# Kernel tuning notes

Hardware: AMD Instinct MI355X
Metric: run time of the kernel (lower is better)

Reference implementation:

```python
import jax, jax.numpy as jnp
import numpy as np

# ---- model hyperparameters (match init_kwargs) ----
N_ATOMS = 16000
N_EDGES = 256000
F = 128          # n_atom_basis
NF = 32          # n_filters
L = 3            # n_interactions
N_RBF = 20
CUTOFF = 5.0
MAX_Z = 100
INV_SQRT_F = np.float32(1.0 / np.sqrt(F))
INV_SQRT_2NF = np.float32(1.0 / np.sqrt(2 * NF))
SQ2 = np.float32(np.sqrt(2.0)); SQ3 = np.float32(np.sqrt(3.0)); SQ6 = np.float32(np.sqrt(6.0))
LOG2 = np.float32(np.log(2.0))


def ssp(x):
    # shifted softplus: softplus(x) - log(2)
    return jax.nn.softplus(x) - LOG2


def setup_inputs() -> dict:
    key = jax.random.key(0)
    k = jax.random.split(key, 16)
    Z = jax.random.randint(k[0], (N_ATOMS,), 0, MAX_Z)
    r_ij = jax.random.normal(k[1], (N_EDGES, 3), dtype=jnp.float32) * 2.0
    idx_i = jnp.sort(jax.random.randint(k[2], (N_EDGES,), 0, N_ATOMS))
    idx_j = jax.random.randint(k[3], (N_EDGES,), 0, N_ATOMS)
    # parameters (e3nn Linear: N(0,1) weights with explicit 1/sqrt(fan_in) in the math;
    # filter-network Dense: fan-in scaled weights, zero bias; padding_idx=0 -> zero row)
    emb = jax.random.normal(k[4], (MAX_Z, F), dtype=jnp.float32).at[0].set(0.0)
    W_pe = jax.random.normal(k[5], (F, F), dtype=jnp.float32)
    W0s = jax.random.normal(k[6], (L, F, NF), dtype=jnp.float32)   # in2f, 0e path
    W0v = jax.random.normal(k[7], (L, F, NF), dtype=jnp.float32)   # in2f, 1o path
    Wf1 = jax.random.normal(k[8], (L, N_RBF, NF), dtype=jnp.float32) / np.sqrt(N_RBF)
    bf1 = jnp.zeros((L, NF), jnp.float32)
    Wf2 = jax.random.normal(k[9], (L, NF, 6 * NF), dtype=jnp.float32) / np.sqrt(NF)
    bf2 = jnp.zeros((L, 6 * NF), jnp.float32)
    As = jax.random.normal(k[10], (L, 2 * NF, F), dtype=jnp.float32)  # f2out_1 0e
    Av = jax.random.normal(k[11], (L, 2 * NF, F), dtype=jnp.float32)  # f2out_1 1o
    Bs = jax.random.normal(k[12], (L, F, F), dtype=jnp.float32)       # f2out_2 0e
    Bv = jax.random.normal(k[13], (L, F, F), dtype=jnp.float32)       # f2out_2 1o
    return dict(Z=Z, r_ij=r_ij, idx_i=idx_i, idx_j=idx_j, emb=emb, W_pe=W_pe,
                W0s=W0s, W0v=W0v, Wf1=Wf1, bf1=bf1, Wf2=Wf2, bf2=bf2,
                As=As, Av=Av, Bs=Bs, Bv=Bv)


def _interaction(xs, xv, idx_i, idx_j, f_ij, rcut, Yv,
                 W0s, W0v, Wf1, bf1, Wf2, bf2, As, Av, Bs, Bv):
    n_atoms = xs.shape[0]
    # in2f: e3nn o3.Linear (per-l channel mixing, fan-in normalized)
    hs = (xs @ W0s) * INV_SQRT_F                        # [N, NF]  (0e)
    hv = jnp.einsum('nfc,fg->ngc', xv, W0v) * INV_SQRT_F  # [N, NF, 3] (1o)
    sj = hs[idx_j]                                      # gather neighbors [E, NF]
    vj = hv[idx_j]                                      # [E, NF, 3]
    # FullTensorProduct (0e+1o) x Y(0e+1o); Y0 = 1, Y1 = sqrt(3)*r_hat (component norm)
    Yb = Yv[:, None, :]                                 # [E, 1, 3]
    t0a = sj                                            # 0e x 0e -> 0e
    t0b = jnp.einsum('efc,ec->ef', vj, Yv) / SQ3        # 1o x 1o -> 0e
    t1a = sj[:, :, None] * Yb                           # 0e x 1o -> 1o
    t1b = vj                                            # 1o x 0e -> 1o
    t1e = jnp.cross(vj, Yb) / SQ2                       # 1o x 1o -> 1e
    ux, uy, uz = vj[..., 0], vj[..., 1], vj[..., 2]
    wx, wy, wz = Yv[:, None, 0], Yv[:, None, 1], Yv[:, None, 2]
    t2e = jnp.stack([(ux * wy + uy * wx) / SQ2,         # 1o x 1o -> 2e (sym traceless)
                     (uy * wz + uz * wy) / SQ2,
                     (2 * uz * wz - ux * wx - uy * wy) / SQ6,
                     (ux * wz + uz * wx) / SQ2,
                     (ux * wx - uy * wy) / SQ2], axis=-1)  # [E, NF, 5]
    # filter network + cutoff envelope: W_ij [E, 6*NF] (one scalar per irrep)
    W = (ssp(f_ij @ Wf1 + bf1) @ Wf2 + bf2) * rcut[:, None]
    w0a, w0b, w1a, w1b, w1e, w2e = jnp.split(W, 6, axis=1)
    E = sj.shape[0]
    # elementwise tensor product (scale each irrep by its scalar), then scatter-add
    y_all = jnp.concatenate([
        t0a * w0a, t0b * w0b,
        (t1a * w1a[..., None]).reshape(E, -1),
        (t1b * w1b[..., None]).reshape(E, -1),
        (t1e * w1e[..., None]).reshape(E, -1),
        (t2e * w2e[..., None]).reshape(E, -1)], axis=1)   # [E, 16*NF]
    agg = jax.ops.segment_sum(y_all, idx_i, num_segments=n_atoms)  # [N, 16*NF]
    s_in = agg[:, :2 * NF]
    v_in = agg[:, 2 * NF:8 * NF].reshape(n_atoms, 2 * NF, 3)
    # f2out_1: output irreps are F x (0e+1o) -> 1e and 2e channels have no path (dropped)
    os = ssp((s_in @ As) * INV_SQRT_2NF)                # f2out_1 + scalar activation
    ov = jnp.einsum('nfc,fg->ngc', v_in, Av) * INV_SQRT_2NF
    os = (os @ Bs) * INV_SQRT_F                         # f2out_2
    ov = jnp.einsum('nfc,fg->ngc', ov, Bv) * INV_SQRT_F
    return os, ov


def _forward(Z, r_ij, idx_i, idx_j, emb, W_pe, W0s, W0v, Wf1, bf1, Wf2, bf2, As, Av, Bs, Bv):
    xs = (emb[Z] @ W_pe) * INV_SQRT_F                   # embedding + post_embedding (0e)
    xv = jnp.zeros((xs.shape[0], F, 3), xs.dtype)       # 1o part starts at zero (no 0e->1o path)
    d = jnp.linalg.norm(r_ij, axis=1)
    offsets = jnp.linspace(0.0, CUTOFF, N_RBF).astype(jnp.float32)
    coeff = -0.5 / (offsets[1] - offsets[0]) ** 2
    f_ij = jnp.exp(coeff * (d[:, None] - offsets) ** 2)  # Gaussian RBF [E, N_RBF]
    rcut = 0.5 * (jnp.cos(np.float32(np.pi) * d / CUTOFF) + 1.0) * (d < CUTOFF)
    # spherical harmonics, normalize=True + component normalization (Y0=1, Y1=sqrt(3)*rhat);
    # the r_ij*rcut prescaling in the original doesn't change the direction, and edges with
    # rcut=0 contribute nothing since W_ij carries the rcut factor.
    Yv = SQ3 * r_ij / jnp.maximum(d, 1e-9)[:, None]
    for l in range(L):
        vs, vv = _interaction(xs, xv, idx_i, idx_j, f_ij, rcut, Yv,
                              W0s[l], W0v[l], Wf1[l], bf1[l], Wf2[l], bf2[l],
                              As[l], Av[l], Bs[l], Bv[l])
        xs = xs + vs
        xv = xv + vv
    return xs  # scalar_representation [N, F]


def reference(Z, r_ij, idx_i, idx_j, emb, W_pe, W0s, W0v, Wf1, bf1, Wf2, bf2, As, Av, Bs, Bv):
    return _forward(Z, r_ij, idx_i, idx_j, emb, W_pe, W0s, W0v, Wf1, bf1, Wf2, bf2, As, Av, Bs, Bv)
```

## Files before the change

### kernel.cpp

```cpp
#include <hip/hip_runtime.h>
#include <math.h>

constexpr int NA   = 16000;
constexpr int NE   = 256000;
constexpr int F    = 128;
constexpr int NF   = 32;
constexpr int NRBF = 20;
constexpr float CUTOFF       = 5.0f;
constexpr float INV_SQRT_F   = 0.0883883476483184f;
constexpr float INV_SQRT_2NF = 0.125f;
constexpr float INV_SQ3      = 0.5773502691896258f;
constexpr float SQ3          = 1.7320508075688772f;
constexpr float LOG2_        = 0.6931471805599453f;
constexpr float PI_          = 3.14159265358979323f;

typedef _Float16 h2 __attribute__((ext_vector_type(2)));

__device__ __forceinline__ float ssp(float x) {
    return fmaxf(x, 0.0f) + __logf(1.0f + __expf(-fabsf(x))) - LOG2_;
}
__device__ __forceinline__ float fdot2(h2 a, h2 b, float c) {
#if __has_builtin(__builtin_amdgcn_fdot2)
    return __builtin_amdgcn_fdot2(a, b, c, false);
#else
    return c + (float)a[0]*(float)b[0] + (float)a[1]*(float)b[1];
#endif
}

__global__ void geom_kernel(const float* __restrict__ r_ij,
                            float* __restrict__ fijT,
                            float* __restrict__ yvrT) {
    int e = blockIdx.x * blockDim.x + threadIdx.x;
    if (e >= NE) return;
    float x = r_ij[3*e+0], y = r_ij[3*e+1], z = r_ij[3*e+2];
    float d = sqrtf(x*x + y*y + z*z);
    const float delta = CUTOFF / (NRBF - 1);
    const float coeff = -0.5f / (delta * delta);
    #pragma unroll
    for (int k = 0; k < NRBF; k++) {
        float t = d - delta * (float)k;
        fijT[(size_t)k*NE + e] = __expf(coeff * t * t);
    }
    float rc = 0.5f * (__cosf(PI_ * d / CUTOFF) + 1.0f);
    rc = (d < CUTOFF) ? rc : 0.0f;
    float inv = SQ3 / fmaxf(d, 1e-9f);
    yvrT[0*(size_t)NE + e] = x * inv;
    yvrT[1*(size_t)NE + e] = y * inv;
    yvrT[2*(size_t)NE + e] = z * inv;
    yvrT[3*(size_t)NE + e] = rc;
}

__global__ void preph_kernel(const float* __restrict__ Wf2, const float* __restrict__ Wf1,
                             h2* __restrict__ Wf2H, h2* __restrict__ Wf1H) {
    int u = blockIdx.x * 256 + threadIdx.x;
    if (u < 3*128*16) {
        int l = u / (128*16), rem = u % (128*16), c = rem >> 4, k2 = rem & 15;
        const float* W = Wf2 + (size_t)l*NF*192;
        Wf2H[u] = h2{(_Float16)W[(2*k2)*192 + c], (_Float16)W[(2*k2+1)*192 + c]};
    }
    if (u < 3*320) {
        int l = u / 320, rem = u % 320, k2 = rem >> 5, g = rem & 31;
        const float* W = Wf1 + (size_t)l*NRBF*NF;
        Wf1H[u] = h2{(_Float16)W[(2*k2)*32 + g], (_Float16)W[(2*k2+1)*32 + g]};
    }
}

__global__ void prep2_kernel(const float* __restrict__ Av, const float* __restrict__ Bv,
                             float* __restrict__ AvBv) {
    int u = blockIdx.x * 256 + threadIdx.x;
    if (u >= 3*64*128) return;
    int l = u >> 13, rem = u & 8191, f = rem >> 7, c = rem & 127;
    const float* av = Av + (size_t)l*64*128 + f*128;
    const float* bv = Bv + (size_t)l*128*128 + c;
    float acc = 0.f;
    #pragma unroll 8
    for (int g = 0; g < 128; g++) acc += av[g] * bv[(size_t)g*128];
    AvBv[u] = acc * (INV_SQRT_2NF * INV_SQRT_F);
}

__global__ __launch_bounds__(256, 4)
void embed_kernel(const int* __restrict__ Z,
                  const float* __restrict__ emb,
                  const float* __restrict__ Wpe,
                  const float* __restrict__ W0s,
                  float* __restrict__ xs,
                  float* __restrict__ hsv) {
    __shared__ float ER[32][128];
    __shared__ int   Zs[32];
    int t = threadIdx.x;
    int a0 = blockIdx.x * 32;
    if (t < 32) Zs[t] = Z[a0 + t];
    __syncthreads();
    {
        const float4* emb4 = (const float4*)emb;
        float4* ER4 = (float4*)&ER[0][0];
        #pragma unroll
        for (int it = 0; it < 4; it++) {
            int u4 = it*256 + t;
            int a = u4 >> 5, k4 = u4 & 31;
            ER4[u4] = emb4[(size_t)Zs[a]*32 + k4];
        }
    }
    __syncthreads();
    int c = t & 127, half = t >> 7;
    float acc[16];
    #pragma unroll
    for (int a = 0; a < 16; a++) acc[a] = 0.f;
    for (int k = 0; k < 128; k++) {
        float w = Wpe[k*128 + c];
        #pragma unroll
        for (int a = 0; a < 16; a++) acc[a] += ER[half*16 + a][k] * w;
    }
    __syncthreads();
    #pragma unroll
    for (int a = 0; a < 16; a++) {
        float v = acc[a] * INV_SQRT_F;
        xs[(size_t)(a0 + half*16 + a)*128 + c] = v;
        ER[half*16 + a][c] = v;
    }
    __syncthreads();
    {
        int g = t & 31, rr = t >> 5;
        float a2[4] = {0.f, 0.f, 0.f, 0.f};
        for (int k = 0; k < 128; k++) {
            float w = W0s[k*32 + g];
            #pragma unroll
            for (int a = 0; a < 4; a++) a2[a] += ER[rr*4 + a][k] * w;
        }
        #pragma unroll
        for (int a = 0; a < 4; a++)
            hsv[(size_t)(a0 + rr*4 + a)*128 + g] = a2[a] * INV_SQRT_F;
        for (int u = t; u < 32*96; u += 256) {
            int a = u / 96, rem = u - a*96;
            hsv[(size_t)(a0 + a)*128 + 32 + rem] = 0.f;
        }
    }
}

__global__ __launch_bounds__(256, 4)
void h_kernel(const float* __restrict__ xs,
              const float* __restrict__ xv,
              const float* __restrict__ W0s,
              const float* __restrict__ W0v,
              float* __restrict__ hsv) {
    __shared__ float X[16][512];
    int t = threadIdx.x;
    int a0 = blockIdx.x * 16;
    {
        float* Xf = &X[0][0];
        const float4* xs4 = (const float4*)xs;
        const float4* xv4 = (const float4*)xv;
        #pragma unroll
        for (int it = 0; it < 2; it++) {
            int u4 = it*256 + t;
            int a = u4 >> 5, k4 = u4 & 31;
            *(float4*)&Xf[a*512 + k4*4] = xs4[(size_t)a0*32 + u4];
        }
        #pragma unroll
        for (int it = 0; it < 6; it++) {
            int u4 = it*256 + t;
            int a = u4 / 96, rem = u4 - a*96;
            *(float4*)&Xf[a*512 + 128 + rem*4] = xv4[(size_t)a0*96 + u4];
        }
    }
    __syncthreads();
    int g = t & 31, r = t >> 5;
    int sel = r & 3, half = r >> 2;
    const float* W = (sel == 0) ? W0s : W0v;
    int xoff = (sel == 0) ? 0 : (128 + (sel-1)*128);
    float acc[8];
    #pragma unroll
    for (int a = 0; a < 8; a++) acc[a] = 0.f;
    for (int k = 0; k < 128; k++) {
        float w = W[k*32 + g];
        #pragma unroll
        for (int a = 0; a < 8; a++) acc[a] += X[half*8 + a][xoff + k] * w;
    }
    #pragma unroll
    for (int a = 0; a < 8; a++) {
        int n = a0 + half*8 + a;
        if (sel == 0) hsv[(size_t)n*128 + g] = acc[a] * INV_SQRT_F;
        else          hsv[(size_t)n*128 + 32 + g*3 + (sel-1)] = acc[a] * INV_SQRT_F;
    }
}

struct alignas(16) HRow { h2 v[20]; };

template <bool DO_V>
__global__ __launch_bounds__(256, 4)
void agg_kernel(const int* __restrict__ idx_i,
                const int* __restrict__ idx_j,
                const float* __restrict__ fijT,
                const float* __restrict__ yvrT,
                const float* __restrict__ hsv,
                const h2* __restrict__ Wf1H,
                const float* __restrict__ bf1,
                const h2* __restrict__ Wf2H,
                const float* __restrict__ bf2,
                float* __restrict__ aggG) {
    __shared__ h2 LW1[320];
    __shared__ HRow HB[4][64];
    int t = threadIdx.x;
    for (int u = t; u < 320; u += 256) LW1[u] = Wf1H[u];
    __syncthreads();

    int wid = t >> 6, lane = t & 63;
    int base = (blockIdx.x*4 + wid) * 64;

    int   il = idx_i[base + lane];
    int   jl = idx_j[base + lane];
    float y0l = yvrT[0*(size_t)NE + base + lane];
    float y1l = yvrT[1*(size_t)NE + base + lane];
    float y2l = yvrT[2*(size_t)NE + base + lane];
    float y3l = yvrT[3*(size_t)NE + base + lane];

    int ilp = __shfl_up(il, 1);
    unsigned long long bmask = __ballot(lane > 0 && il != ilp);

    h2 fp[10];
    #pragma unroll
    for (int k2 = 0; k2 < 10; k2++) {
        float fa = fijT[(size_t)(2*k2)*NE + base + lane];
        float fb = fijT[(size_t)(2*k2+1)*NE + base + lane];
        fp[k2] = h2{(_Float16)fa, (_Float16)fb};
    }
    float h[32];
    #pragma unroll
    for (int g = 0; g < 32; g++) h[g] = bf1[g];
    #pragma unroll
    for (int k2 = 0; k2 < 10; k2++) {
        #pragma unroll
        for (int g = 0; g < 32; g++)
            h[g] = fdot2(fp[k2], LW1[k2*32 + g], h[g]);
    }
    #pragma unroll
    for (int g = 0; g < 32; g++) h[g] = ssp(h[g]);
    {
        h2 hp[16];
        #pragma unroll
        for (int i = 0; i < 16; i++) hp[i] = h2{(_Float16)h[2*i], (_Float16)h[2*i+1]};
        float4* dst = (float4*)HB[wid][lane].v;
        const float4* srcp = (const float4*)hp;
        #pragma unroll
        for (int w = 0; w < 4; w++) dst[w] = srcp[w];
    }

    h2 w2a[16], w2b[16];
    #pragma unroll
    for (int k2 = 0; k2 < 16; k2++) {
        w2a[k2] = Wf2H[lane*16 + k2];
        asm volatile("" : "+v"(w2a[k2]));
    }
    if (DO_V) {
        #pragma unroll
        for (int k2 = 0; k2 < 16; k2++) {
            w2b[k2] = Wf2H[(64+lane)*16 + k2];
            asm volatile("" : "+v"(w2b[k2]));
        }
    }
    float bf2a = bf2[lane];
    float bf2b = DO_V ? bf2[64 + lane] : 0.f;

    int idxQ = 32 + 3*(lane - 32);
    int off0 = (lane < 32) ? lane : idxQ;
    int off1 = (lane < 32) ? lane : (idxQ + 1);
    int off2 = (lane < 32) ? lane : (idxQ + 2);

    float a0 = 0.f, a1 = 0.f, a2 = 0.f, a3 = 0.f;
    int prev = __builtin_amdgcn_readlane(il, 0);

    float qn0, qn1, qn2;
    float4 hbn[4];
    {
        int j = __builtin_amdgcn_readlane(jl, 0);
        const float* row = hsv + (size_t)j*128;
        qn0 = row[off0]; qn1 = row[off1]; qn2 = row[off2];
        const float4* hq4 = (const float4*)HB[wid][0].v;
        hbn[0] = hq4[0]; hbn[1] = hq4[1]; hbn[2] = hq4[2]; hbn[3] = hq4[3];
    }
    for (int ii = 0; ii < 64; ++ii) {
        float q0 = qn0, q1 = qn1, q2 = qn2;
        float4 hbc[4] = { hbn[0], hbn[1], hbn[2], hbn[3] };
        if (ii < 63) {
            int j = __builtin_amdgcn_readlane(jl, ii + 1);
            const float* row = hsv + (size_t)j*128;
            qn0 = row[off0]; qn1 = row[off1]; qn2 = row[off2];
            const float4* hq4 = (const float4*)HB[wid][ii + 1].v;
            hbn[0] = hq4[0]; hbn[1] = hq4[1]; hbn[2] = hq4[2]; hbn[3] = hq4[3];
        }
        if ((bmask >> ii) & 1ull) {
            unsafeAtomicAdd(&aggG[(size_t)prev*256 + lane], a0);
            a0 = 0.f;
            if (DO_V) {
                unsafeAtomicAdd(&aggG[(size_t)prev*256 + 64 + lane],  a1);
                unsafeAtomicAdd(&aggG[(size_t)prev*256 + 128 + lane], a2);
                unsafeAtomicAdd(&aggG[(size_t)prev*256 + 192 + lane], a3);
                a1 = a2 = a3 = 0.f;
            }
            prev = __builtin_amdgcn_readlane(il, ii);
        }
        float s0 = bf2a, s1 = bf2b;
        {
            const h2* hh = (const h2*)hbc;
            #pragma unroll
            for (int k2 = 0; k2 < 16; k2++) {
                s0 = fdot2(hh[k2], w2a[k2], s0);
                if (DO_V) s1 = fdot2(hh[k2], w2b[k2], s1);
            }
        }
        float y3s = __int_as_float(__builtin_amdgcn_readlane(__float_as_int(y3l), ii));
        float y0s = __int_as_float(__builtin_amdgcn_readlane(__float_as_int(y0l), ii));
        float y1s = __int_as_float(__builtin_amdgcn_readlane(__float_as_int(y1l), ii));
        float y2s = __int_as_float(__builtin_amdgcn_readlane(__float_as_int(y2l), ii));
        float w0 = s0 * y3s;
        float dot = (q0*y0s + q1*y1s + q2*y2s) * INV_SQ3;
        float v0 = (lane < 32) ? q0 : dot;
        a0 += v0 * w0;
        if (DO_V) {
            float w1 = s1 * y3s;
            float m1 = (lane < 32) ? y0s : 1.0f;
            float m2 = (lane < 32) ? y1s : 1.0f;
            float m3 = (lane < 32) ? y2s : 1.0f;
            a1 += q0 * m1 * w1;
            a2 += q1 * m2 * w1;
            a3 += q2 * m3 * w1;
        }
    }
    unsafeAtomicAdd(&aggG[(size_t)prev*256 + lane], a0);
    if (DO_V) {
        unsafeAtomicAdd(&aggG[(size_t)prev*256 + 64 + lane],  a1);
        unsafeAtomicAdd(&aggG[(size_t)prev*256 + 128 + lane], a2);
        unsafeAtomicAdd(&aggG[(size_t)prev*256 + 192 + lane], a3);
    }
}

template <bool DO_V, bool XV_WRITE, bool ZERO_AGG>
__global__ __launch_bounds__(256, 4)
void mlp_kernel(const float* __restrict__ aggG,
                const float* __restrict__ As,
                const float* __restrict__ Bs,
                const float* __restrict__ AvBv,
                float* __restrict__ xs,
                float* __restrict__ xv,
                float* __restrict__ aggW) {
    constexpr int AC = DO_V ? 256 : 64;
    __shared__ float aggL[16][AC];
    __shared__ float outL[16][128];
    int t = threadIdx.x;
    int a0 = blockIdx.x * 16;
    {
        const float4* g4 = (const float4*)(aggG + (size_t)a0*256);
        if (DO_V) {
            float4* l4 = (float4*)&aggL[0][0];
            #pragma unroll
            for (int it = 0; it < 4; it++) l4[it*256 + t] = g4[it*256 + t];
        } else {
            int row = t >> 4, c4 = t & 15;
            *(float4*)&aggL[row][c4*4] = g4[row*64 + c4];
        }
    }
    __syncthreads();
    if (ZERO_AGG) {
        float4 z = make_float4(0.f, 0.f, 0.f, 0.f);
        float4* g4w = (float4*)(aggW + (size_t)a0*256);
        #pragma unroll
        for (int it = 0; it < 4; it++) g4w[it*256 + t] = z;
    }

    int q  = t & 31;
    int rp = t >> 5;
    const float4* As4 = (const float4*)As;
    const float4* Bs4 = (const float4*)Bs;

    {
        float ox0=0,oy0=0,oz0=0,ow0=0, ox1=0,oy1=0,oz1=0,ow1=0;
        const float4* x0p = (const float4*)&aggL[rp][0];
        const float4* x1p = (const float4*)&aggL[rp+8][0];
        #pragma unroll 4
        for (int kq = 0; kq < 16; kq++) {
            float4 x0 = x0p[kq], x1 = x1p[kq];
            float4 wa = As4[(4*kq+0)*32 + q];
            float4 wb = As4[(4*kq+1)*32 + q];
            float4 wc = As4[(4*kq+2)*32 + q];
            float4 wd = As4[(4*kq+3)*32 + q];
            ox0 += x0.x*wa.x + x0.y*wb.x + x0.z*wc.x + x0.w*wd.x;
            oy0 += x0.x*wa.y + x0.y*wb.y + x0.z*wc.y + x0.w*wd.y;
            oz0 += x0.x*wa.z + x0.y*wb.z + x0.z*wc.z + x0.w*wd.z;
            ow0 += x0.x*wa.w + x0.y*wb.w + x0.z*wc.w + x0.w*wd.w;
            ox1 += x1.x*wa.x + x1.y*wb.x + x1.z*wc.x + x1.w*wd.x;
            oy1 += x1.x*wa.y + x1.y*wb.y + x1.z*wc.y + x1.w*wd.y;
            oz1 += x1.x*wa.z + x1.y*wb.z + x1.z*wc.z + x1.w*wd.z;
            ow1 += x1.x*wa.w + x1.y*wb.w + x1.z*wc.w + x1.w*wd.w;
        }
        float4 r0 = { ssp(ox0*INV_SQRT_2NF), ssp(oy0*INV_SQRT_2NF), ssp(oz0*INV_SQRT_2NF), ssp(ow0*INV_SQRT_2NF) };
        float4 r1 = { ssp(ox1*INV_SQRT_2NF), ssp(oy1*INV_SQRT_2NF), ssp(oz1*INV_SQRT_2NF), ssp(ow1*INV_SQRT_2NF) };
        *(float4*)&outL[rp][4*q]   = r0;
        *(float4*)&outL[rp+8][4*q] = r1;
    }
    if (DO_V) {
        const float4* AB4 = (const float4*)AvBv;
        int ra[6], rc[6];
        #pragma unroll
        for (int i = 0; i < 6; i++) {
            int rv = rp + 8*i;
            ra[i] = rv/3; rc[i] = rv - 3*(rv/3);
        }
        float o[6][4];
        #pragma unroll
        for (int i = 0; i < 6; i++) { o[i][0]=0; o[i][1]=0; o[i][2]=0; o[i][3]=0; }
        const float4* vp[6];
        #pragma unroll
        for (int i = 0; i < 6; i++)
            vp[i] = (const float4*)&aggL[ra[i]][64 + rc[i]*64];
        #pragma unroll 2
        for (int kq = 0; kq < 16; kq++) {
            float4 wa = AB4[(4*kq+0)*32 + q];
            float4 wb = AB4[(4*kq+1)*32 + q];
            float4 wc = AB4[(4*kq+2)*32 + q];
            float4 wd = AB4[(4*kq+3)*32 + q];
            #pragma unroll
            for (int i = 0; i < 6; i++) {
                float4 x = vp[i][kq];
                o[i][0] += x.x*wa.x + x.y*wb.x + x.z*wc.x + x.w*wd.x;
                o[i][1] += x.x*wa.y + x.y*wb.y + x.z*wc.y + x.w*wd.y;
                o[i][2] += x.x*wa.z + x.y*wb.z + x.z*wc.z + x.w*wd.z;
                o[i][3] += x.x*wa.w + x.y*wb.w + x.z*wc.w + x.w*wd.w;
            }
        }
        #pragma unroll
        for (int i = 0; i < 6; i++) {
            float4* p = (float4*)&xv[(size_t)(a0+ra[i])*384 + rc[i]*128 + 4*q];
            if (XV_WRITE) {
                float4 c = make_float4(o[i][0], o[i][1], o[i][2], o[i][3]);
                *p = c;
            } else {
                float4 c = *p;
                c.x += o[i][0]; c.y += o[i][1]; c.z += o[i][2]; c.w += o[i][3];
                *p = c;
            }
        }
    }
    __syncthreads();
    {
        float ox0=0,oy0=0,oz0=0,ow0=0, ox1=0,oy1=0,oz1=0,ow1=0;
        const float4* x0p = (const float4*)&outL[rp][0];
        const float4* x1p = (const float4*)&outL[rp+8][0];
        #pragma unroll 4
        for (int kq = 0; kq < 32; kq++) {
            float4 x0 = x0p[kq], x1 = x1p[kq];
            float4 wa = Bs4[(4*kq+0)*32 + q];
            float4 wb = Bs4[(4*kq+1)*32 + q];
            float4 wc = Bs4[(4*kq+2)*32 + q];
            float4 wd = Bs4[(4*kq+3)*32 + q];
            ox0 += x0.x*wa.x + x0.y*wb.x + x0.z*wc.x + x0.w*wd.x;
            oy0 += x0.x*wa.y + x0.y*wb.y + x0.z*wc.y + x0.w*wd.y;
            oz0 += x0.x*wa.z + x0.y*wb.z + x0.z*wc.z + x0.w*wd.z;
            ow0 += x0.x*wa.w + x0.y*wb.w + x0.z*wc.w + x0.w*wd.w;
            ox1 += x1.x*wa.x + x1.y*wb.x + x1.z*wc.x + x1.w*wd.x;
            oy1 += x1.x*wa.y + x1.y*wb.y + x1.z*wc.y + x1.w*wd.y;
            oz1 += x1.x*wa.z + x1.y*wb.z + x1.z*wc.z + x1.w*wd.z;
            ow1 += x1.x*wa.w + x1.y*wb.w + x1.z*wc.w + x1.w*wd.w;
        }
        float4* p0 = (float4*)&xs[(size_t)(a0+rp)*128 + 4*q];
        float4* p1 = (float4*)&xs[(size_t)(a0+rp+8)*128 + 4*q];
        float4 c0 = *p0, c1 = *p1;
        c0.x += ox0*INV_SQRT_F; c0.y += oy0*INV_SQRT_F; c0.z += oz0*INV_SQRT_F; c0.w += ow0*INV_SQRT_F;
        c1.x += ox1*INV_SQRT_F; c1.y += oy1*INV_SQRT_F; c1.z += oz1*INV_SQRT_F; c1.w += ow1*INV_SQRT_F;
        *p0 = c0; *p1 = c1;
    }
}

extern "C" void kernel_launch(void* const* d_in, const int* in_sizes, int n_in,
                              void* d_out, int out_size, void* d_ws, size_t ws_size,
                              hipStream_t stream) {
    (void)in_sizes; (void)n_in; (void)out_size; (void)ws_size;
    const int*   Z     = (const int*)  d_in[0];
    const float* r_ij  = (const float*)d_in[1];
    const int*   idx_i = (const int*)  d_in[2];
    const int*   idx_j = (const int*)  d_in[3];
    const float* emb   = (const float*)d_in[4];
    const float* Wpe   = (const float*)d_in[5];
    const float* W0s   = (const float*)d_in[6];
    const float* W0v   = (const float*)d_in[7];
    const float* Wf1   = (const float*)d_in[8];
    const float* bf1   = (const float*)d_in[9];
    const float* Wf2   = (const float*)d_in[10];
    const float* bf2   = (const float*)d_in[11];
    const float* As    = (const float*)d_in[12];
    const float* Av    = (const float*)d_in[13];
    const float* Bs    = (const float*)d_in[14];
    const float* Bv    = (const float*)d_in[15];

    float* xs = (float*)d_out;
    float* ws = (float*)d_ws;
    float* fijT = ws;
    float* yvrT = fijT + (size_t)NE*NRBF;
    float* xv   = yvrT + (size_t)NE*4;
    float* hsv  = xv   + (size_t)NA*F*3;
    float* aggG = hsv  + (size_t)NA*F;
    float* AvBv = aggG + (size_t)NA*256;
    h2*    Wf2H = (h2*)(AvBv + (size_t)3*64*128);
    h2*    Wf1H = Wf2H + (size_t)3*128*16;

    geom_kernel<<<(NE+255)/256, 256, 0, stream>>>(r_ij, fijT, yvrT);
    preph_kernel<<<24, 256, 0, stream>>>(Wf2, Wf1, Wf2H, Wf1H);
    prep2_kernel<<<(3*64*128+255)/256, 256, 0, stream>>>(Av, Bv, AvBv);
    embed_kernel<<<NA/32, 256, 0, stream>>>(Z, emb, Wpe, W0s, xs, hsv);
    hipMemsetAsync(aggG, 0, (size_t)NA*256*sizeof(float), stream);

    for (int l = 0; l < 3; l++) {
        if (l > 0)
            h_kernel<<<NA/16, 256, 0, stream>>>(xs, xv,
                W0s + (size_t)l*F*NF, W0v + (size_t)l*F*NF, hsv);

        if (l < 2)
            agg_kernel<true><<<NE/256, 256, 0, stream>>>(idx_i, idx_j, fijT, yvrT, hsv,
                Wf1H + (size_t)l*320, bf1 + (size_t)l*NF,
                Wf2H + (size_t)l*128*16, bf2 + (size_t)l*6*NF, aggG);
        else
            agg_kernel<false><<<NE/256, 256, 0, stream>>>(idx_i, idx_j, fijT, yvrT, hsv,
                Wf1H + (size_t)l*320, bf1 + (size_t)l*NF,
                Wf2H + (size_t)l*128*16, bf2 + (size_t)l*6*NF, aggG);

        if (l == 0)
            mlp_kernel<true, true, true><<<NA/16, 256, 0, stream>>>(aggG,
                As + (size_t)l*2*NF*F, Bs + (size_t)l*F*F, AvBv + (size_t)l*64*128,
                xs, xv, aggG);
        else if (l == 1)
            mlp_kernel<true, false, true><<<NA/16, 256, 0, stream>>>(aggG,
                As + (size_t)l*2*NF*F, Bs + (size_t)l*F*F, AvBv + (size_t)l*64*128,
                xs, xv, aggG);
        else
            mlp_kernel<false, false, false><<<NA/16, 256, 0, stream>>>(aggG,
                As + (size_t)l*2*NF*F, Bs + (size_t)l*F*F, AvBv + (size_t)l*64*128,
                xs, xv, aggG);
    }
}
```

Measured before the change: 357.4 us.

## Halve edges per wave in agg kernel and split filter MLP across wave halves

Each wave now handles 32 edges instead of 64. The two wave halves each compute 16 of the 32 first-layer filter outputs for the same edge, which halves the per-thread h register array. Launch bounds go from 4 to 8 waves per SIMD, the shared HB buffer shrinks, and the grid doubles. The aim is more occupancy and shorter serial per-edge loops, at the cost of more blocks, twice as many atomic flushes at segment boundaries, and more redundant weight loads per edge.

```diff
diff --git a/kernel.cpp b/kernel.cpp
--- a/kernel.cpp
+++ b/kernel.cpp
@@ -184,10 +184,10 @@
     }
 }
 
-struct alignas(16) HRow { h2 v[20]; };
+struct alignas(16) HRow { h2 v[16]; };
 
 template <bool DO_V>
-__global__ __launch_bounds__(256, 4)
+__global__ __launch_bounds__(256, 8)
 void agg_kernel(const int* __restrict__ idx_i,
                 const int* __restrict__ idx_j,
                 const float* __restrict__ fijT,
@@ -199,50 +199,52 @@
                 const float* __restrict__ bf2,
                 float* __restrict__ aggG) {
     __shared__ h2 LW1[320];
-    __shared__ HRow HB[4][64];
+    __shared__ HRow HB[4][32];
     int t = threadIdx.x;
     for (int u = t; u < 320; u += 256) LW1[u] = Wf1H[u];
     __syncthreads();
 
     int wid = t >> 6, lane = t & 63;
-    int base = (blockIdx.x*4 + wid) * 64;
-
-    int   il = idx_i[base + lane];
-    int   jl = idx_j[base + lane];
-    float y0l = yvrT[0*(size_t)NE + base + lane];
-    float y1l = yvrT[1*(size_t)NE + base + lane];
-    float y2l = yvrT[2*(size_t)NE + base + lane];
-    float y3l = yvrT[3*(size_t)NE + base + lane];
+    int base = (blockIdx.x*4 + wid) * 32;
+    int eL  = lane & 31;
+    int selH = lane >> 5;
+
+    int   il = idx_i[base + eL];
+    int   jl = idx_j[base + eL];
+    float y0l = yvrT[0*(size_t)NE + base + eL];
+    float y1l = yvrT[1*(size_t)NE + base + eL];
+    float y2l = yvrT[2*(size_t)NE + base + eL];
+    float y3l = yvrT[3*(size_t)NE + base + eL];
 
     int ilp = __shfl_up(il, 1);
-    unsigned long long bmask = __ballot(lane > 0 && il != ilp);
+    unsigned long long bmask = __ballot(lane > 0 && lane < 32 && il != ilp);
 
     h2 fp[10];
     #pragma unroll
     for (int k2 = 0; k2 < 10; k2++) {
-        float fa = fijT[(size_t)(2*k2)*NE + base + lane];
-        float fb = fijT[(size_t)(2*k2+1)*NE + base + lane];
+        float fa = fijT[(size_t)(2*k2)*NE + base + eL];
+        float fb = fijT[(size_t)(2*k2+1)*NE + base + eL];
         fp[k2] = h2{(_Float16)fa, (_Float16)fb};
     }
-    float h[32];
-    #pragma unroll
-    for (int g = 0; g < 32; g++) h[g] = bf1[g];
-    #pragma unroll
-    for (int k2 = 0; k2 < 10; k2++) {
-        #pragma unroll
-        for (int g = 0; g < 32; g++)
-            h[g] = fdot2(fp[k2], LW1[k2*32 + g], h[g]);
-    }
-    #pragma unroll
-    for (int g = 0; g < 32; g++) h[g] = ssp(h[g]);
-    {
-        h2 hp[16];
-        #pragma unroll
-        for (int i = 0; i < 16; i++) hp[i] = h2{(_Float16)h[2*i], (_Float16)h[2*i+1]};
-        float4* dst = (float4*)HB[wid][lane].v;
+    {
+        float h[16];
+        #pragma unroll
+        for (int gg = 0; gg < 16; gg++) h[gg] = bf1[selH*16 + gg];
+        #pragma unroll
+        for (int k2 = 0; k2 < 10; k2++) {
+            #pragma unroll
+            for (int gg = 0; gg < 16; gg++)
+                h[gg] = fdot2(fp[k2], LW1[k2*32 + selH*16 + gg], h[gg]);
+        }
+        #pragma unroll
+        for (int gg = 0; gg < 16; gg++) h[gg] = ssp(h[gg]);
+        h2 hp[8];
+        #pragma unroll
+        for (int i = 0; i < 8; i++) hp[i] = h2{(_Float16)h[2*i], (_Float16)h[2*i+1]};
+        float4* dst = (float4*)&HB[wid][eL].v[selH*8];
         const float4* srcp = (const float4*)hp;
-        #pragma unroll
-        for (int w = 0; w < 4; w++) dst[w] = srcp[w];
+        dst[0] = srcp[0];
+        dst[1] = srcp[1];
     }
 
     h2 w2a[16], w2b[16];
@@ -278,10 +280,10 @@
         const float4* hq4 = (const float4*)HB[wid][0].v;
         hbn[0] = hq4[0]; hbn[1] = hq4[1]; hbn[2] = hq4[2]; hbn[3] = hq4[3];
     }
-    for (int ii = 0; ii < 64; ++ii) {
+    for (int ii = 0; ii < 32; ++ii) {
         float q0 = qn0, q1 = qn1, q2 = qn2;
         float4 hbc[4] = { hbn[0], hbn[1], hbn[2], hbn[3] };
-        if (ii < 63) {
+        if (ii < 31) {
             int j = __builtin_amdgcn_readlane(jl, ii + 1);
             const float* row = hsv + (size_t)j*128;
             qn0 = row[off0]; qn1 = row[off1]; qn2 = row[off2];
@@ -514,11 +516,11 @@
                 W0s + (size_t)l*F*NF, W0v + (size_t)l*F*NF, hsv);
 
         if (l < 2)
-            agg_kernel<true><<<NE/256, 256, 0, stream>>>(idx_i, idx_j, fijT, yvrT, hsv,
+            agg_kernel<true><<<NE/128, 256, 0, stream>>>(idx_i, idx_j, fijT, yvrT, hsv,
                 Wf1H + (size_t)l*320, bf1 + (size_t)l*NF,
                 Wf2H + (size_t)l*128*16, bf2 + (size_t)l*6*NF, aggG);
         else
-            agg_kernel<false><<<NE/256, 256, 0, stream>>>(idx_i, idx_j, fijT, yvrT, hsv,
+            agg_kernel<false><<<NE/128, 256, 0, stream>>>(idx_i, idx_j, fijT, yvrT, hsv,
                 Wf1H + (size_t)l*320, bf1 + (size_t)l*NF,
                 Wf2H + (size_t)l*128*16, bf2 + (size_t)l*6*NF, aggG);
 
```

New measurement: 960.9 us. 2.69x slower.
